# Kernel tuning notes

Measured on AMD Instinct MI355X. Metric: run time of the kernel, lower is better.

Reference implementation:

```python
import jax, jax.numpy as jnp
import numpy as np

TOKENS, IN_F, OUT_F = 8192, 4096, 4096

def setup_inputs() -> dict:
    key = jax.random.key(0)
    k1, k2, k3, k4 = jax.random.split(key, 4)
    # int8 activations and weights in [-127, 127]
    x = jax.random.randint(k1, (TOKENS, IN_F), -127, 128, dtype=jnp.int32).astype(jnp.int8)
    weight = jax.random.randint(k2, (OUT_F, IN_F), -127, 128, dtype=jnp.int32).astype(jnp.int8)  # [out, in]
    # static per-output-channel dequant scale (fp16), small so fp16 output doesn't overflow
    dequant_scale = (jax.random.uniform(k3, (OUT_F,), dtype=jnp.float32) * 1e-3).astype(jnp.float16)
    bias = (jax.random.normal(k4, (OUT_F,), dtype=jnp.float32)).astype(jnp.float16)
    return {"x": x, "weight": weight, "dequant_scale": dequant_scale, "bias": bias}

def reference(x, weight, dequant_scale, bias):
    # int8 GEMM with int32 accumulation: [tokens, in] @ [in, out] -> [tokens, out]
    acc = jax.lax.dot_general(
        x, weight.T,
        dimension_numbers=(((1,), (0,)), ((), ())),
        preferred_element_type=jnp.int32,
    )
    # static per-output-channel dequant, cast to fp16, add fp16 bias
    out = (acc.astype(jnp.float32) * dequant_scale.astype(jnp.float32)[None, :]).astype(jnp.float16)
    out = out + bias[None, :]
    # module returns (output, output_bias)
    return (out, bias)
```

## Files before the change

### kernel.cpp

```cpp
#include <hip/hip_runtime.h>
#include <hip/hip_fp16.h>
#include <stdint.h>

typedef __attribute__((ext_vector_type(4))) int int32x4;
typedef __attribute__((ext_vector_type(4))) float float32x4;

#define TOKENS 8192
#define IN_F   4096
#define OUT_F  4096
#define BM 256
#define BN 256
#define BK 128
#define NT (IN_F / BK)
#define ESTR 260

#define AS1 __attribute__((address_space(1)))
#define AS3 __attribute__((address_space(3)))

__global__ __launch_bounds__(256)
void pack_all_kernel(const int* __restrict__ x32, const int* __restrict__ w32,
                     const float* __restrict__ bias,
                     uint32_t* __restrict__ x8, uint32_t* __restrict__ w8,
                     float* __restrict__ bias_out)
{
    const int gid = blockIdx.x * 256 + threadIdx.x;
    if (gid < OUT_F / 4) {
        float32x4 b4 = __builtin_nontemporal_load((const float32x4*)bias + gid);
        __builtin_nontemporal_store(b4, (float32x4*)bias_out + gid);
    }

    const int nx4 = TOKENS * IN_F / 4;
    const int nw4 = OUT_F * IN_F / 4;
    for (int i = gid; i < nx4 + nw4; i += gridDim.x * 256) {
        const int* s; uint32_t* d; int j;
        if (i < nx4) { s = x32; d = x8; j = i; }
        else         { s = w32; d = w8; j = i - nx4; }
        int32x4 v = __builtin_nontemporal_load((const int32x4*)s + j);
        d[j] = (uint32_t)(v[0] & 0xff) | ((uint32_t)(v[1] & 0xff) << 8) |
               ((uint32_t)(v[2] & 0xff) << 16) | ((uint32_t)v[3] << 24);
    }
}

__global__ __launch_bounds__(512, 2)
void w8a8_gemm_kernel(const int8_t* __restrict__ x,
                      const int8_t* __restrict__ w,
                      const float* __restrict__ scale,
                      const float* __restrict__ bias,
                      float* __restrict__ out)
{
    __shared__ int8_t smem[131072];
    int8_t* lA = smem;
    int8_t* lB = smem + 65536;

    const int tid = threadIdx.x;
    const int wv  = tid >> 6;
    const int l   = tid & 63;
    const int wqm = wv >> 1;
    const int wqn = wv & 1;

    const int xc  = blockIdx.x & 7;
    const int idx = blockIdx.x >> 3;
    const int bn  = (xc & 1) * 8 + (idx & 7);
    const int bm  = (xc >> 1) * 8 + (idx >> 3);

    const int8_t* baseA = x + (size_t)bm * BM * IN_F;
    const int8_t* baseB = w + (size_t)bn * BN * IN_F;

    const int seg0 = wv * 2, seg1 = wv * 2 + 1;
    const int r8   = l >> 3;
    const int swc  = (((l & 7) ^ r8) << 4);

    const int8_t* pA0 = baseA + (size_t)(seg0 * 8 + r8) * IN_F + swc;
    const int8_t* pA1 = baseA + (size_t)(seg1 * 8 + r8) * IN_F + swc;
    const int8_t* pB0 = baseB + (size_t)(seg0 * 8 + r8) * IN_F + swc;
    const int8_t* pB1 = baseB + (size_t)(seg1 * 8 + r8) * IN_F + swc;

    const int fr  = l & 15;
    const int xk  = (l & 7) << 4;
    const int cb0 = (l >> 4) << 4;

    int32x4 acc[2][2][2][4];
#pragma unroll
    for (int a0 = 0; a0 < 2; ++a0)
#pragma unroll
        for (int a1 = 0; a1 < 2; ++a1)
#pragma unroll
            for (int a2 = 0; a2 < 2; ++a2)
#pragma unroll
                for (int a3 = 0; a3 < 4; ++a3)
                    acc[a0][a1][a2][a3] = (int32x4){0, 0, 0, 0};

    int32x4 aF[2][2][2];
    int32x4 bF[2][4][2];

    auto stage_half = [&](int h4) {
        const int kt_ = h4 >> 2;
        const int wh_ = h4 & 3;
        const size_t off = (size_t)(wh_ & 1) * (128 * IN_F) + (size_t)kt_ * BK;
        const int8_t* s0 = ((wh_ < 2) ? pA0 : pB0) + off;
        const int8_t* s1 = ((wh_ < 2) ? pA1 : pB1) + off;
        int8_t* db = ((wh_ < 2) ? lA : lB) + ((kt_ & 1) << 15) + ((wh_ & 1) << 14);
        __builtin_amdgcn_global_load_lds(
            (const AS1 void*)s0, (AS3 void*)(db + seg0 * 1024), 16, 0, 0);
        __builtin_amdgcn_global_load_lds(
            (const AS1 void*)s1, (AS3 void*)(db + seg1 * 1024), 16, 0, 0);
    };

#define LDA(MH)                                                                        \
    do {                                                                               \
        _Pragma("unroll") for (int mi = 0; mi < 2; ++mi)                               \
        _Pragma("unroll") for (int ks = 0; ks < 2; ++ks)                               \
            aF[MH][mi][ks] = *(const int32x4*)&lAb[((MH) << 14) +                      \
                (wqm * 32 + mi * 16 + fr) * 128 + (((ks * 64) + cb0) ^ xk)];           \
    } while (0)

#define LDB(NH)                                                                        \
    do {                                                                               \
        _Pragma("unroll") for (int ni = 0; ni < 4; ++ni)                               \
        _Pragma("unroll") for (int ks = 0; ks < 2; ++ks)                               \
            bF[NH][ni][ks] = *(const int32x4*)&lBb[((NH) << 14) +                      \
                (wqn * 64 + ni * 16 + fr) * 128 + (((ks * 64) + cb0) ^ xk)];           \
    } while (0)

#define MMAQ(MH, NH)                                                                   \
    do {                                                                               \
        _Pragma("unroll") for (int mi = 0; mi < 2; ++mi)                               \
        _Pragma("unroll") for (int ni = 0; ni < 4; ++ni)                               \
        _Pragma("unroll") for (int ks = 0; ks < 2; ++ks)                               \
            acc[MH][NH][mi][ni] = __builtin_amdgcn_mfma_i32_16x16x64_i8(               \
                aF[MH][mi][ks], bF[NH][ni][ks], acc[MH][NH][mi][ni], 0, 0, 0);         \
    } while (0)

    stage_half(0); stage_half(1); stage_half(2); stage_half(3);
    asm volatile("s_waitcnt vmcnt(0)" ::: "memory");
    __builtin_amdgcn_s_barrier();

    for (int t = 0; t < NT; ++t) {
        const int8_t* lAb = lA + ((t & 1) << 15);
        const int8_t* lBb = lB + ((t & 1) << 15);

        LDA(0); LDB(0); LDB(1); LDA(1);

        if (t + 1 < NT) {
            stage_half(4 * (t + 1) + 0); stage_half(4 * (t + 1) + 1);
            stage_half(4 * (t + 1) + 2); stage_half(4 * (t + 1) + 3);
        }

        __builtin_amdgcn_s_setprio(1);
        MMAQ(0, 0); MMAQ(0, 1); MMAQ(1, 0); MMAQ(1, 1);
        __builtin_amdgcn_s_setprio(0);

        if (t + 1 < NT) asm volatile("s_waitcnt vmcnt(0)" ::: "memory");
        __builtin_amdgcn_s_barrier();
    }

    __syncthreads();
    int* eL = (int*)smem;
    const int c4   = tid & 63;
    const int rowt = tid >> 6;
    const float32x4 sc4 = ((const float32x4*)scale)[bn * 64 + c4];
    const float32x4 bf4 = ((const float32x4*)bias )[bn * 64 + c4];
    const __half bh[4] = { __float2half(bf4[0]), __float2half(bf4[1]),
                           __float2half(bf4[2]), __float2half(bf4[3]) };
    const int r0 = (l >> 4) << 2;
    const int wr0 = (wqm & 1) * 32 + r0;

    for (int c = 0; c < 4; ++c) {
        if ((wqm >> 1) == (c & 1)) {
            const int MH = c >> 1;
#pragma unroll
            for (int NH = 0; NH < 2; ++NH)
#pragma unroll
                for (int mi = 0; mi < 2; ++mi)
#pragma unroll
                    for (int ni = 0; ni < 4; ++ni)
#pragma unroll
                        for (int r = 0; r < 4; ++r)
                            eL[(wr0 + mi * 16 + r) * ESTR +
                               NH * 128 + wqn * 64 + ni * 16 + fr] = acc[MH][NH][mi][ni][r];
        }
        __syncthreads();
#pragma unroll
        for (int p = 0; p < 8; ++p) {
            const int rl = p * 8 + rowt;
            int32x4 v = *(const int32x4*)&eL[rl * ESTR + c4 * 4];
            float32x4 o;
#pragma unroll
            for (int j = 0; j < 4; ++j) {
                __half h = __float2half((float)v[j] * sc4[j]);
                o[j] = __half2float(__hadd(h, bh[j]));
            }
            const size_t rowg = (size_t)(bm * 256 + c * 64 + rl);
            __builtin_nontemporal_store(o, (float32x4*)out + rowg * (OUT_F / 4) + bn * 64 + c4);
        }
        __syncthreads();
    }
#undef LDA
#undef LDB
#undef MMAQ
}

extern "C" void kernel_launch(void* const* d_in, const int* in_sizes, int n_in,
                              void* d_out, int out_size, void* d_ws, size_t ws_size,
                              hipStream_t stream)
{
    const int*   x32   = (const int*)d_in[0];
    const int*   w32   = (const int*)d_in[1];
    const float* scale = (const float*)d_in[2];
    const float* bias  = (const float*)d_in[3];
    float* out = (float*)d_out;

    int8_t* x8 = (int8_t*)d_ws;
    int8_t* w8 = x8 + (size_t)TOKENS * IN_F;

    pack_all_kernel<<<3072, 256, 0, stream>>>(x32, w32, bias, (uint32_t*)x8, (uint32_t*)w8,
                                              out + (size_t)TOKENS * OUT_F);

    w8a8_gemm_kernel<<<512, 512, 0, stream>>>(x8, w8, scale, bias, out);
}
```

Baseline: 185.9 us.

## Load B fragments directly from global into registers, keep only A in LDS

The weight operand now skips LDS staging. Each lane loads its MFMA B fragments straight from global memory into registers, double-buffered across the two k-halves. LDS use drops from 128KB to 64KB, which removes the B LDS reads and may raise occupancy. In exchange it issues many more uncoalesced 16-byte global loads per wave with no reuse across waves. The epilogue is reworked into 8 chunks of 32 rows to match the new layout.

New measurement: 338.4 us. 82.0% more time.

```diff
diff --git a/kernel.cpp b/kernel.cpp
--- a/kernel.cpp
+++ b/kernel.cpp
@@ -43,14 +43,13 @@
 
 __global__ __launch_bounds__(512, 2)
 void w8a8_gemm_kernel(const int8_t* __restrict__ x,
-                      const int8_t* __restrict__ w,
+                      const int8_t* __restrict__ wq,
                       const float* __restrict__ scale,
                       const float* __restrict__ bias,
                       float* __restrict__ out)
 {
-    __shared__ int8_t smem[131072];
+    __shared__ int8_t smem[65536];
     int8_t* lA = smem;
-    int8_t* lB = smem + 65536;
 
     const int tid = threadIdx.x;
     const int wv  = tid >> 6;
@@ -64,93 +63,91 @@
     const int bm  = (xc >> 1) * 8 + (idx >> 3);
 
     const int8_t* baseA = x + (size_t)bm * BM * IN_F;
-    const int8_t* baseB = w + (size_t)bn * BN * IN_F;
 
     const int seg0 = wv * 2, seg1 = wv * 2 + 1;
     const int r8   = l >> 3;
     const int swc  = (((l & 7) ^ r8) << 4);
-
     const int8_t* pA0 = baseA + (size_t)(seg0 * 8 + r8) * IN_F + swc;
     const int8_t* pA1 = baseA + (size_t)(seg1 * 8 + r8) * IN_F + swc;
-    const int8_t* pB0 = baseB + (size_t)(seg0 * 8 + r8) * IN_F + swc;
-    const int8_t* pB1 = baseB + (size_t)(seg1 * 8 + r8) * IN_F + swc;
 
     const int fr  = l & 15;
     const int xk  = (l & 7) << 4;
     const int cb0 = (l >> 4) << 4;
 
+    const int8_t* pB = wq + (size_t)(bn * 256 + wqn * 64 + fr) * IN_F + ((l >> 4) << 4);
+
     int32x4 acc[2][2][2][4];
 #pragma unroll
-    for (int a0 = 0; a0 < 2; ++a0)
-#pragma unroll
-        for (int a1 = 0; a1 < 2; ++a1)
-#pragma unroll
-            for (int a2 = 0; a2 < 2; ++a2)
-#pragma unroll
-                for (int a3 = 0; a3 < 4; ++a3)
-                    acc[a0][a1][a2][a3] = (int32x4){0, 0, 0, 0};
+    for (int a0i = 0; a0i < 2; ++a0i)
+#pragma unroll
+        for (int a1i = 0; a1i < 2; ++a1i)
+#pragma unroll
+            for (int a2i = 0; a2i < 2; ++a2i)
+#pragma unroll
+                for (int a3i = 0; a3i < 4; ++a3i)
+                    acc[a0i][a1i][a2i][a3i] = (int32x4){0, 0, 0, 0};
 
     int32x4 aF[2][2][2];
-    int32x4 bF[2][4][2];
-
-    auto stage_half = [&](int h4) {
-        const int kt_ = h4 >> 2;
-        const int wh_ = h4 & 3;
-        const size_t off = (size_t)(wh_ & 1) * (128 * IN_F) + (size_t)kt_ * BK;
-        const int8_t* s0 = ((wh_ < 2) ? pA0 : pB0) + off;
-        const int8_t* s1 = ((wh_ < 2) ? pA1 : pB1) + off;
-        int8_t* db = ((wh_ < 2) ? lA : lB) + ((kt_ & 1) << 15) + ((wh_ & 1) << 14);
-        __builtin_amdgcn_global_load_lds(
-            (const AS1 void*)s0, (AS3 void*)(db + seg0 * 1024), 16, 0, 0);
-        __builtin_amdgcn_global_load_lds(
-            (const AS1 void*)s1, (AS3 void*)(db + seg1 * 1024), 16, 0, 0);
+    int32x4 bK0[2][4];
+    int32x4 bK1[2][4];
+
+    auto stage_A = [&](int t) {
+        int8_t* db = lA + ((t & 1) << 15);
+        const size_t co = (size_t)t * BK;
+        __builtin_amdgcn_global_load_lds((const AS1 void*)(pA0 + co),
+                                         (AS3 void*)(db + seg0 * 1024), 16, 0, 0);
+        __builtin_amdgcn_global_load_lds((const AS1 void*)(pA1 + co),
+                                         (AS3 void*)(db + seg1 * 1024), 16, 0, 0);
+        __builtin_amdgcn_global_load_lds((const AS1 void*)(pA0 + 128 * IN_F + co),
+                                         (AS3 void*)(db + 16384 + seg0 * 1024), 16, 0, 0);
+        __builtin_amdgcn_global_load_lds((const AS1 void*)(pA1 + 128 * IN_F + co),
+                                         (AS3 void*)(db + 16384 + seg1 * 1024), 16, 0, 0);
     };
 
-#define LDA(MH)                                                                        \
+#define LDA_ALL(LABP)                                                                  \
     do {                                                                               \
+        _Pragma("unroll") for (int MH = 0; MH < 2; ++MH)                               \
         _Pragma("unroll") for (int mi = 0; mi < 2; ++mi)                               \
         _Pragma("unroll") for (int ks = 0; ks < 2; ++ks)                               \
-            aF[MH][mi][ks] = *(const int32x4*)&lAb[((MH) << 14) +                      \
+            aF[MH][mi][ks] = *(const int32x4*)&(LABP)[(MH << 14) +                     \
                 (wqm * 32 + mi * 16 + fr) * 128 + (((ks * 64) + cb0) ^ xk)];           \
     } while (0)
 
-#define LDB(NH)                                                                        \
+#define LDBG(DST, T, KS)                                                               \
     do {                                                                               \
+        _Pragma("unroll") for (int NH = 0; NH < 2; ++NH)                               \
         _Pragma("unroll") for (int ni = 0; ni < 4; ++ni)                               \
-        _Pragma("unroll") for (int ks = 0; ks < 2; ++ks)                               \
-            bF[NH][ni][ks] = *(const int32x4*)&lBb[((NH) << 14) +                      \
-                (wqn * 64 + ni * 16 + fr) * 128 + (((ks * 64) + cb0) ^ xk)];           \
+            DST[NH][ni] = *(const int32x4*)(pB +                                       \
+                (size_t)(NH * 128 + ni * 16) * IN_F + (T) * 128 + (KS) * 64);          \
     } while (0)
 
-#define MMAQ(MH, NH)                                                                   \
+#define MMAK(KS, BSET)                                                                 \
     do {                                                                               \
+        _Pragma("unroll") for (int MH = 0; MH < 2; ++MH)                               \
+        _Pragma("unroll") for (int NH = 0; NH < 2; ++NH)                               \
         _Pragma("unroll") for (int mi = 0; mi < 2; ++mi)                               \
         _Pragma("unroll") for (int ni = 0; ni < 4; ++ni)                               \
-        _Pragma("unroll") for (int ks = 0; ks < 2; ++ks)                               \
             acc[MH][NH][mi][ni] = __builtin_amdgcn_mfma_i32_16x16x64_i8(               \
-                aF[MH][mi][ks], bF[NH][ni][ks], acc[MH][NH][mi][ni], 0, 0, 0);         \
+                aF[MH][mi][KS], BSET[NH][ni], acc[MH][NH][mi][ni], 0, 0, 0);           \
     } while (0)
 
-    stage_half(0); stage_half(1); stage_half(2); stage_half(3);
+    stage_A(0);
+    LDBG(bK0, 0, 0);
     asm volatile("s_waitcnt vmcnt(0)" ::: "memory");
     __builtin_amdgcn_s_barrier();
 
     for (int t = 0; t < NT; ++t) {
         const int8_t* lAb = lA + ((t & 1) << 15);
-        const int8_t* lBb = lB + ((t & 1) << 15);
-
-        LDA(0); LDB(0); LDB(1); LDA(1);
-
-        if (t + 1 < NT) {
-            stage_half(4 * (t + 1) + 0); stage_half(4 * (t + 1) + 1);
-            stage_half(4 * (t + 1) + 2); stage_half(4 * (t + 1) + 3);
-        }
-
-        __builtin_amdgcn_s_setprio(1);
-        MMAQ(0, 0); MMAQ(0, 1); MMAQ(1, 0); MMAQ(1, 1);
-        __builtin_amdgcn_s_setprio(0);
-
-        if (t + 1 < NT) asm volatile("s_waitcnt vmcnt(0)" ::: "memory");
+
+        LDA_ALL(lAb);
+        if (t + 1 < NT) stage_A(t + 1);
+        LDBG(bK1, t, 1);
+
+        MMAK(0, bK0);
+        if (t + 1 < NT) LDBG(bK0, t + 1, 0);
+        MMAK(1, bK1);
+
+        asm volatile("s_waitcnt vmcnt(0)" ::: "memory");
         __builtin_amdgcn_s_barrier();
     }
 
@@ -163,11 +160,10 @@
     const __half bh[4] = { __float2half(bf4[0]), __float2half(bf4[1]),
                            __float2half(bf4[2]), __float2half(bf4[3]) };
     const int r0 = (l >> 4) << 2;
-    const int wr0 = (wqm & 1) * 32 + r0;
-
-    for (int c = 0; c < 4; ++c) {
-        if ((wqm >> 1) == (c & 1)) {
-            const int MH = c >> 1;
+
+    for (int c = 0; c < 8; ++c) {
+        if (wqm == (c & 3)) {
+            const int MH = c >> 2;
 #pragma unroll
             for (int NH = 0; NH < 2; ++NH)
 #pragma unroll
@@ -176,12 +172,12 @@
                     for (int ni = 0; ni < 4; ++ni)
 #pragma unroll
                         for (int r = 0; r < 4; ++r)
-                            eL[(wr0 + mi * 16 + r) * ESTR +
+                            eL[(mi * 16 + r0 + r) * ESTR +
                                NH * 128 + wqn * 64 + ni * 16 + fr] = acc[MH][NH][mi][ni][r];
         }
         __syncthreads();
 #pragma unroll
-        for (int p = 0; p < 8; ++p) {
+        for (int p = 0; p < 4; ++p) {
             const int rl = p * 8 + rowt;
             int32x4 v = *(const int32x4*)&eL[rl * ESTR + c4 * 4];
             float32x4 o;
@@ -190,14 +186,14 @@
                 __half h = __float2half((float)v[j] * sc4[j]);
                 o[j] = __half2float(__hadd(h, bh[j]));
             }
-            const size_t rowg = (size_t)(bm * 256 + c * 64 + rl);
+            const size_t rowg = (size_t)(bm * 256 + c * 32 + rl);
             __builtin_nontemporal_store(o, (float32x4*)out + rowg * (OUT_F / 4) + bn * 64 + c4);
         }
         __syncthreads();
     }
-#undef LDA
-#undef LDB
-#undef MMAQ
+#undef LDA_ALL
+#undef LDBG
+#undef MMAK
 }
 
 extern "C" void kernel_launch(void* const* d_in, const int* in_sizes, int n_in,
```

## Switch int8 GEMM from 16x16x64 to 32x32x32 MFMA tiles

Applied to the files above, without the earlier changes.

Replaces the 16x16x64 int8 MFMA with the 32x32x32 variant. Fragment loads, accumulator layout and the epilogue's LDS staging are reworked to match the 32x32 output layout. The larger MFMA tile reuses each operand fragment over more output elements, cutting LDS read traffic per MAC and the instruction count. In exchange the epilogue makes more passes with more barriers, and register pressure and LDS bank-conflict behaviour change.

Result: slower. 210.8 us (+13.4%).

```diff
diff --git a/kernel.cpp b/kernel.cpp
--- a/kernel.cpp
+++ b/kernel.cpp
@@ -2,8 +2,9 @@
 #include <hip/hip_fp16.h>
 #include <stdint.h>
 
-typedef __attribute__((ext_vector_type(4))) int int32x4;
-typedef __attribute__((ext_vector_type(4))) float float32x4;
+typedef __attribute__((ext_vector_type(4)))  int int32x4;
+typedef __attribute__((ext_vector_type(16))) int int32x16;
+typedef __attribute__((ext_vector_type(4)))  float float32x4;
 
 #define TOKENS 8192
 #define IN_F   4096
@@ -43,7 +44,7 @@
 
 __global__ __launch_bounds__(512, 2)
 void w8a8_gemm_kernel(const int8_t* __restrict__ x,
-                      const int8_t* __restrict__ w,
+                      const int8_t* __restrict__ wq,
                       const float* __restrict__ scale,
                       const float* __restrict__ bias,
                       float* __restrict__ out)
@@ -64,34 +65,33 @@
     const int bm  = (xc >> 1) * 8 + (idx >> 3);
 
     const int8_t* baseA = x + (size_t)bm * BM * IN_F;
-    const int8_t* baseB = w + (size_t)bn * BN * IN_F;
+    const int8_t* baseB = wq + (size_t)bn * BN * IN_F;
 
     const int seg0 = wv * 2, seg1 = wv * 2 + 1;
     const int r8   = l >> 3;
     const int swc  = (((l & 7) ^ r8) << 4);
-
     const int8_t* pA0 = baseA + (size_t)(seg0 * 8 + r8) * IN_F + swc;
     const int8_t* pA1 = baseA + (size_t)(seg1 * 8 + r8) * IN_F + swc;
     const int8_t* pB0 = baseB + (size_t)(seg0 * 8 + r8) * IN_F + swc;
     const int8_t* pB1 = baseB + (size_t)(seg1 * 8 + r8) * IN_F + swc;
 
-    const int fr  = l & 15;
+    const int r32 = l & 31;
+    const int kh  = (l >> 5) << 4;
     const int xk  = (l & 7) << 4;
-    const int cb0 = (l >> 4) << 4;
-
-    int32x4 acc[2][2][2][4];
-#pragma unroll
-    for (int a0 = 0; a0 < 2; ++a0)
-#pragma unroll
-        for (int a1 = 0; a1 < 2; ++a1)
-#pragma unroll
-            for (int a2 = 0; a2 < 2; ++a2)
-#pragma unroll
-                for (int a3 = 0; a3 < 4; ++a3)
-                    acc[a0][a1][a2][a3] = (int32x4){0, 0, 0, 0};
-
-    int32x4 aF[2][2][2];
-    int32x4 bF[2][4][2];
+
+    int32x16 acc[2][2][2];
+#pragma unroll
+    for (int a0i = 0; a0i < 2; ++a0i)
+#pragma unroll
+        for (int a1i = 0; a1i < 2; ++a1i)
+#pragma unroll
+            for (int a2i = 0; a2i < 2; ++a2i)
+#pragma unroll
+                for (int e = 0; e < 16; ++e)
+                    acc[a0i][a1i][a2i][e] = 0;
+
+    int32x4 aF[2][4];
+    int32x4 bF[2][2][4];
 
     auto stage_half = [&](int h4) {
         const int kt_ = h4 >> 2;
@@ -106,29 +106,31 @@
             (const AS1 void*)s1, (AS3 void*)(db + seg1 * 1024), 16, 0, 0);
     };
 
-#define LDA(MH)                                                                        \
+#define LDA_ALL(LABP)                                                                  \
     do {                                                                               \
-        _Pragma("unroll") for (int mi = 0; mi < 2; ++mi)                               \
-        _Pragma("unroll") for (int ks = 0; ks < 2; ++ks)                               \
-            aF[MH][mi][ks] = *(const int32x4*)&lAb[((MH) << 14) +                      \
-                (wqm * 32 + mi * 16 + fr) * 128 + (((ks * 64) + cb0) ^ xk)];           \
+        _Pragma("unroll") for (int MH = 0; MH < 2; ++MH)                               \
+        _Pragma("unroll") for (int kb = 0; kb < 4; ++kb)                               \
+            aF[MH][kb] = *(const int32x4*)&(LABP)[(MH << 14) +                         \
+                (wqm * 32 + r32) * 128 + (((kb * 32) + kh) ^ xk)];                     \
     } while (0)
 
-#define LDB(NH)                                                                        \
+#define LDB_ALL(LBBP)                                                                  \
     do {                                                                               \
-        _Pragma("unroll") for (int ni = 0; ni < 4; ++ni)                               \
-        _Pragma("unroll") for (int ks = 0; ks < 2; ++ks)                               \
-            bF[NH][ni][ks] = *(const int32x4*)&lBb[((NH) << 14) +                      \
-                (wqn * 64 + ni * 16 + fr) * 128 + (((ks * 64) + cb0) ^ xk)];           \
+        _Pragma("unroll") for (int NH = 0; NH < 2; ++NH)                               \
+        _Pragma("unroll") for (int cb = 0; cb < 2; ++cb)                               \
+        _Pragma("unroll") for (int kb = 0; kb < 4; ++kb)                               \
+            bF[NH][cb][kb] = *(const int32x4*)&(LBBP)[(NH << 14) +                     \
+                (wqn * 64 + cb * 32 + r32) * 128 + (((kb * 32) + kh) ^ xk)];           \
     } while (0)
 
-#define MMAQ(MH, NH)                                                                   \
+#define MMA_ALL()                                                                      \
     do {                                                                               \
-        _Pragma("unroll") for (int mi = 0; mi < 2; ++mi)                               \
-        _Pragma("unroll") for (int ni = 0; ni < 4; ++ni)                               \
-        _Pragma("unroll") for (int ks = 0; ks < 2; ++ks)                               \
-            acc[MH][NH][mi][ni] = __builtin_amdgcn_mfma_i32_16x16x64_i8(               \
-                aF[MH][mi][ks], bF[NH][ni][ks], acc[MH][NH][mi][ni], 0, 0, 0);         \
+        _Pragma("unroll") for (int MH = 0; MH < 2; ++MH)                               \
+        _Pragma("unroll") for (int NH = 0; NH < 2; ++NH)                               \
+        _Pragma("unroll") for (int cb = 0; cb < 2; ++cb)                               \
+        _Pragma("unroll") for (int kb = 0; kb < 4; ++kb)                               \
+            acc[MH][NH][cb] = __builtin_amdgcn_mfma_i32_32x32x32_i8(                   \
+                aF[MH][kb], bF[NH][cb][kb], acc[MH][NH][cb], 0, 0, 0);                 \
     } while (0)
 
     stage_half(0); stage_half(1); stage_half(2); stage_half(3);
@@ -139,7 +141,7 @@
         const int8_t* lAb = lA + ((t & 1) << 15);
         const int8_t* lBb = lB + ((t & 1) << 15);
 
-        LDA(0); LDB(0); LDB(1); LDA(1);
+        LDA_ALL(lAb); LDB_ALL(lBb);
 
         if (t + 1 < NT) {
             stage_half(4 * (t + 1) + 0); stage_half(4 * (t + 1) + 1);
@@ -147,7 +149,7 @@
         }
 
         __builtin_amdgcn_s_setprio(1);
-        MMAQ(0, 0); MMAQ(0, 1); MMAQ(1, 0); MMAQ(1, 1);
+        MMA_ALL();
         __builtin_amdgcn_s_setprio(0);
 
         if (t + 1 < NT) asm volatile("s_waitcnt vmcnt(0)" ::: "memory");
@@ -162,26 +164,25 @@
     const float32x4 bf4 = ((const float32x4*)bias )[bn * 64 + c4];
     const __half bh[4] = { __float2half(bf4[0]), __float2half(bf4[1]),
                            __float2half(bf4[2]), __float2half(bf4[3]) };
-    const int r0 = (l >> 4) << 2;
-    const int wr0 = (wqm & 1) * 32 + r0;
-
-    for (int c = 0; c < 4; ++c) {
-        if ((wqm >> 1) == (c & 1)) {
-            const int MH = c >> 1;
+    const int rbase = (l >> 5) << 2;
+
+    for (int c = 0; c < 8; ++c) {
+        if (wqm == (c & 3)) {
+            const int MH = c >> 2;
 #pragma unroll
             for (int NH = 0; NH < 2; ++NH)
 #pragma unroll
-                for (int mi = 0; mi < 2; ++mi)
-#pragma unroll
-                    for (int ni = 0; ni < 4; ++ni)
-#pragma unroll
-                        for (int r = 0; r < 4; ++r)
-                            eL[(wr0 + mi * 16 + r) * ESTR +
-                               NH * 128 + wqn * 64 + ni * 16 + fr] = acc[MH][NH][mi][ni][r];
+                for (int cb = 0; cb < 2; ++cb)
+#pragma unroll
+                    for (int j = 0; j < 16; ++j) {
+                        const int rr = (j & 3) + 8 * (j >> 2) + rbase;
+                        eL[rr * ESTR + NH * 128 + wqn * 64 + cb * 32 + r32] =
+                            acc[MH][NH][cb][j];
+                    }
         }
         __syncthreads();
 #pragma unroll
-        for (int p = 0; p < 8; ++p) {
+        for (int p = 0; p < 4; ++p) {
             const int rl = p * 8 + rowt;
             int32x4 v = *(const int32x4*)&eL[rl * ESTR + c4 * 4];
             float32x4 o;
@@ -190,14 +191,14 @@
                 __half h = __float2half((float)v[j] * sc4[j]);
                 o[j] = __half2float(__hadd(h, bh[j]));
             }
-            const size_t rowg = (size_t)(bm * 256 + c * 64 + rl);
+            const size_t rowg = (size_t)(bm * 256 + c * 32 + rl);
             __builtin_nontemporal_store(o, (float32x4*)out + rowg * (OUT_F / 4) + bn * 64 + c4);
         }
         __syncthreads();
     }
-#undef LDA
-#undef LDB
-#undef MMAQ
+#undef LDA_ALL
+#undef LDB_ALL
+#undef MMA_ALL
 }
 
 extern "C" void kernel_launch(void* const* d_in, const int* in_sizes, int n_in,
```

## Use 4 waves with 128x128 per-wave tiles instead of 8 waves

Applied to the files above, without the earlier changes.

Halves the workgroup to 256 threads (4 waves) so each wave computes a 128x128 output sub-tile with 8x8 MFMA accumulators. Fragment loads are split per 64-wide k-slice, and global-to-LDS staging is reorganised so each wave issues four loads per half-tile. The aim is a higher MFMA-to-LDS-read ratio per wave. In exchange it needs 256 accumulator registers per lane, occupancy drops to one block of 4 waves, and the setprio hints are removed. The epilogue is reworked into eight 32-row chunks.

After: 254.2 us. +36.7%, slower.

```diff
diff --git a/kernel.cpp b/kernel.cpp
--- a/kernel.cpp
+++ b/kernel.cpp
@@ -41,9 +41,9 @@
     }
 }
 
-__global__ __launch_bounds__(512, 2)
+__global__ __launch_bounds__(256, 1)
 void w8a8_gemm_kernel(const int8_t* __restrict__ x,
-                      const int8_t* __restrict__ w,
+                      const int8_t* __restrict__ wq,
                       const float* __restrict__ scale,
                       const float* __restrict__ bias,
                       float* __restrict__ out)
@@ -64,74 +64,63 @@
     const int bm  = (xc >> 1) * 8 + (idx >> 3);
 
     const int8_t* baseA = x + (size_t)bm * BM * IN_F;
-    const int8_t* baseB = w + (size_t)bn * BN * IN_F;
-
-    const int seg0 = wv * 2, seg1 = wv * 2 + 1;
+    const int8_t* baseB = wq + (size_t)bn * BN * IN_F;
+
     const int r8   = l >> 3;
     const int swc  = (((l & 7) ^ r8) << 4);
-
-    const int8_t* pA0 = baseA + (size_t)(seg0 * 8 + r8) * IN_F + swc;
-    const int8_t* pA1 = baseA + (size_t)(seg1 * 8 + r8) * IN_F + swc;
-    const int8_t* pB0 = baseB + (size_t)(seg0 * 8 + r8) * IN_F + swc;
-    const int8_t* pB1 = baseB + (size_t)(seg1 * 8 + r8) * IN_F + swc;
+    const int8_t* pA = baseA + (size_t)(wv * 32 + r8) * IN_F + swc;
+    const int8_t* pB = baseB + (size_t)(wv * 32 + r8) * IN_F + swc;
 
     const int fr  = l & 15;
     const int xk  = (l & 7) << 4;
     const int cb0 = (l >> 4) << 4;
 
-    int32x4 acc[2][2][2][4];
-#pragma unroll
-    for (int a0 = 0; a0 < 2; ++a0)
-#pragma unroll
-        for (int a1 = 0; a1 < 2; ++a1)
-#pragma unroll
-            for (int a2 = 0; a2 < 2; ++a2)
-#pragma unroll
-                for (int a3 = 0; a3 < 4; ++a3)
-                    acc[a0][a1][a2][a3] = (int32x4){0, 0, 0, 0};
-
-    int32x4 aF[2][2][2];
-    int32x4 bF[2][4][2];
+    int32x4 acc[8][8];
+#pragma unroll
+    for (int mi = 0; mi < 8; ++mi)
+#pragma unroll
+        for (int ni = 0; ni < 8; ++ni)
+            acc[mi][ni] = (int32x4){0, 0, 0, 0};
+
+    int32x4 aF[8], bF[8];
 
     auto stage_half = [&](int h4) {
         const int kt_ = h4 >> 2;
         const int wh_ = h4 & 3;
         const size_t off = (size_t)(wh_ & 1) * (128 * IN_F) + (size_t)kt_ * BK;
-        const int8_t* s0 = ((wh_ < 2) ? pA0 : pB0) + off;
-        const int8_t* s1 = ((wh_ < 2) ? pA1 : pB1) + off;
-        int8_t* db = ((wh_ < 2) ? lA : lB) + ((kt_ & 1) << 15) + ((wh_ & 1) << 14);
-        __builtin_amdgcn_global_load_lds(
-            (const AS1 void*)s0, (AS3 void*)(db + seg0 * 1024), 16, 0, 0);
-        __builtin_amdgcn_global_load_lds(
-            (const AS1 void*)s1, (AS3 void*)(db + seg1 * 1024), 16, 0, 0);
+        const int8_t* s = ((wh_ < 2) ? pA : pB) + off;
+        int8_t* db = ((wh_ < 2) ? lA : lB) + ((kt_ & 1) << 15) + ((wh_ & 1) << 14)
+                     + wv * 4096;
+#pragma unroll
+        for (int i = 0; i < 4; ++i)
+            __builtin_amdgcn_global_load_lds(
+                (const AS1 void*)(s + (size_t)(i * 8) * IN_F),
+                (AS3 void*)(db + i * 1024), 16, 0, 0);
     };
-
-#define LDA(MH)                                                                        \
+    auto stage_tile = [&](int tt) {
+        stage_half(4 * tt + 0); stage_half(4 * tt + 1);
+        stage_half(4 * tt + 2); stage_half(4 * tt + 3);
+    };
+
+#define LDFR(KS, LABP, LBBP)                                                           \
     do {                                                                               \
-        _Pragma("unroll") for (int mi = 0; mi < 2; ++mi)                               \
-        _Pragma("unroll") for (int ks = 0; ks < 2; ++ks)                               \
-            aF[MH][mi][ks] = *(const int32x4*)&lAb[((MH) << 14) +                      \
-                (wqm * 32 + mi * 16 + fr) * 128 + (((ks * 64) + cb0) ^ xk)];           \
+        _Pragma("unroll") for (int mi = 0; mi < 8; ++mi)                               \
+            aF[mi] = *(const int32x4*)&(LABP)[(wqm << 14) +                            \
+                (mi * 16 + fr) * 128 + ((((KS) * 64) + cb0) ^ xk)];                    \
+        _Pragma("unroll") for (int ni = 0; ni < 8; ++ni)                               \
+            bF[ni] = *(const int32x4*)&(LBBP)[(wqn << 14) +                            \
+                (ni * 16 + fr) * 128 + ((((KS) * 64) + cb0) ^ xk)];                    \
     } while (0)
 
-#define LDB(NH)                                                                        \
+#define MMA64()                                                                        \
     do {                                                                               \
-        _Pragma("unroll") for (int ni = 0; ni < 4; ++ni)                               \
-        _Pragma("unroll") for (int ks = 0; ks < 2; ++ks)                               \
-            bF[NH][ni][ks] = *(const int32x4*)&lBb[((NH) << 14) +                      \
-                (wqn * 64 + ni * 16 + fr) * 128 + (((ks * 64) + cb0) ^ xk)];           \
+        _Pragma("unroll") for (int mi = 0; mi < 8; ++mi)                               \
+        _Pragma("unroll") for (int ni = 0; ni < 8; ++ni)                               \
+            acc[mi][ni] = __builtin_amdgcn_mfma_i32_16x16x64_i8(                       \
+                aF[mi], bF[ni], acc[mi][ni], 0, 0, 0);                                 \
     } while (0)
 
-#define MMAQ(MH, NH)                                                                   \
-    do {                                                                               \
-        _Pragma("unroll") for (int mi = 0; mi < 2; ++mi)                               \
-        _Pragma("unroll") for (int ni = 0; ni < 4; ++ni)                               \
-        _Pragma("unroll") for (int ks = 0; ks < 2; ++ks)                               \
-            acc[MH][NH][mi][ni] = __builtin_amdgcn_mfma_i32_16x16x64_i8(               \
-                aF[MH][mi][ks], bF[NH][ni][ks], acc[MH][NH][mi][ni], 0, 0, 0);         \
-    } while (0)
-
-    stage_half(0); stage_half(1); stage_half(2); stage_half(3);
+    stage_tile(0);
     asm volatile("s_waitcnt vmcnt(0)" ::: "memory");
     __builtin_amdgcn_s_barrier();
 
@@ -139,16 +128,12 @@
         const int8_t* lAb = lA + ((t & 1) << 15);
         const int8_t* lBb = lB + ((t & 1) << 15);
 
-        LDA(0); LDB(0); LDB(1); LDA(1);
-
-        if (t + 1 < NT) {
-            stage_half(4 * (t + 1) + 0); stage_half(4 * (t + 1) + 1);
-            stage_half(4 * (t + 1) + 2); stage_half(4 * (t + 1) + 3);
-        }
-
-        __builtin_amdgcn_s_setprio(1);
-        MMAQ(0, 0); MMAQ(0, 1); MMAQ(1, 0); MMAQ(1, 1);
-        __builtin_amdgcn_s_setprio(0);
+        LDFR(0, lAb, lBb);
+        if (t + 1 < NT) stage_tile(t + 1);
+        MMA64();
+
+        LDFR(1, lAb, lBb);
+        MMA64();
 
         if (t + 1 < NT) asm volatile("s_waitcnt vmcnt(0)" ::: "memory");
         __builtin_amdgcn_s_barrier();
@@ -163,26 +148,23 @@
     const __half bh[4] = { __float2half(bf4[0]), __float2half(bf4[1]),
                            __float2half(bf4[2]), __float2half(bf4[3]) };
     const int r0 = (l >> 4) << 2;
-    const int wr0 = (wqm & 1) * 32 + r0;
-
-    for (int c = 0; c < 4; ++c) {
-        if ((wqm >> 1) == (c & 1)) {
-            const int MH = c >> 1;
-#pragma unroll
-            for (int NH = 0; NH < 2; ++NH)
-#pragma unroll
-                for (int mi = 0; mi < 2; ++mi)
-#pragma unroll
-                    for (int ni = 0; ni < 4; ++ni)
-#pragma unroll
-                        for (int r = 0; r < 4; ++r)
-                            eL[(wr0 + mi * 16 + r) * ESTR +
-                               NH * 128 + wqn * 64 + ni * 16 + fr] = acc[MH][NH][mi][ni][r];
+
+    for (int c = 0; c < 8; ++c) {
+        if (wqm == (c >> 2)) {
+            const int mb = (c & 3) * 2;
+#pragma unroll
+            for (int mi2 = 0; mi2 < 2; ++mi2)
+#pragma unroll
+                for (int ni = 0; ni < 8; ++ni)
+#pragma unroll
+                    for (int r = 0; r < 4; ++r)
+                        eL[(mi2 * 16 + r0 + r) * ESTR +
+                           wqn * 128 + ni * 16 + fr] = acc[mb + mi2][ni][r];
         }
         __syncthreads();
 #pragma unroll
         for (int p = 0; p < 8; ++p) {
-            const int rl = p * 8 + rowt;
+            const int rl = p * 4 + rowt;
             int32x4 v = *(const int32x4*)&eL[rl * ESTR + c4 * 4];
             float32x4 o;
 #pragma unroll
@@ -190,14 +172,13 @@
                 __half h = __float2half((float)v[j] * sc4[j]);
                 o[j] = __half2float(__hadd(h, bh[j]));
             }
-            const size_t rowg = (size_t)(bm * 256 + c * 64 + rl);
+            const size_t rowg = (size_t)(bm * 256 + c * 32 + rl);
             __builtin_nontemporal_store(o, (float32x4*)out + rowg * (OUT_F / 4) + bn * 64 + c4);
         }
         __syncthreads();
     }
-#undef LDA
-#undef LDB
-#undef MMAQ
+#undef LDFR
+#undef MMA64
 }
 
 extern "C" void kernel_launch(void* const* d_in, const int* in_sizes, int n_in,
@@ -216,5 +197,5 @@
     pack_all_kernel<<<3072, 256, 0, stream>>>(x32, w32, bias, (uint32_t*)x8, (uint32_t*)w8,
                                               out + (size_t)TOKENS * OUT_F);
 
-    w8a8_gemm_kernel<<<512, 512, 0, stream>>>(x8, w8, scale, bias, out);
+    w8a8_gemm_kernel<<<512, 256, 0, stream>>>(x8, w8, scale, bias, out);
 }
```
